# Kernel tuning notes

Hardware: AMD Instinct MI355X
Metric: run time of the kernel (lower is better)

## Reference

```python
import jax, jax.numpy as jnp
import numpy as np

VOCAB = 50257
EMB = 256
HID = 256
FORGET_BIAS = 1.0


def setup_inputs() -> dict:
    key = jax.random.key(0)
    ks = jax.random.split(key, 8)
    B, T = 16, 256
    s = 0.05
    return {
        "tokens": jax.random.randint(ks[0], (B, T), 0, VOCAB, dtype=jnp.int32),
        # embedding matrix init mimics tf.random_uniform(-1, 1)
        "emb": jax.random.uniform(ks[1], (VOCAB, EMB), jnp.float32, -1.0, 1.0),
        "W1": jax.random.normal(ks[2], (EMB + HID, 4 * HID), jnp.float32) * s,
        "b1": jnp.zeros((4 * HID,), jnp.float32),
        "W2": jax.random.normal(ks[3], (HID + HID, 4 * HID), jnp.float32) * s,
        "b2": jnp.zeros((4 * HID,), jnp.float32),
        "Wout": jax.random.normal(ks[4], (HID, VOCAB), jnp.float32) * s,
        "bout": jnp.zeros((VOCAB,), jnp.float32),
    }


def _lstm_cell(c, h, x, W, b):
    # BasicLSTMCell: gates = [x, h] @ W + b, split i, j, f, o
    g = jnp.concatenate([x, h], axis=-1) @ W + b
    i, j, f, o = jnp.split(g, 4, axis=-1)
    c_new = c * jax.nn.sigmoid(f + FORGET_BIAS) + jax.nn.sigmoid(i) * jnp.tanh(j)
    h_new = jnp.tanh(c_new) * jax.nn.sigmoid(o)
    return c_new, h_new


def reference(tokens, emb, W1, b1, W2, b2, Wout, bout):
    B, T = tokens.shape
    x = emb[tokens]                 # [B, T, EMB] embedding lookup
    x_tm = jnp.swapaxes(x, 0, 1)    # [T, B, EMB] time-major for scan

    def step(carry, xt):
        c1, h1, c2, h2 = carry
        c1, h1 = _lstm_cell(c1, h1, xt, W1, b1)
        c2, h2 = _lstm_cell(c2, h2, h1, W2, b2)
        return (c1, h1, c2, h2), h2

    z = jnp.zeros((B, HID), x.dtype)
    _, hs = jax.lax.scan(step, (z, z, z, z), x_tm)  # hs: [T, B, HID]
    hs = jnp.swapaxes(hs, 0, 1).reshape(-1, HID)    # [B*T, HID] (batch-major flatten as in tf.reshape)
    logits = hs @ Wout + bout                        # [B*T, VOCAB]
    return logits
```

## Files before the change

### kernel.cpp

```cpp
#include <hip/hip_runtime.h>
#include <hip/hip_bf16.h>
#include <stdint.h>

#define BB 16
#define TT 256
#define HH 256
#define EE 256
#define GG 1024
#define VV 50257
#define NN 4096

typedef unsigned short u16;
typedef __attribute__((ext_vector_type(8))) short short8;
typedef __attribute__((ext_vector_type(4))) float f32x4;

__device__ __forceinline__ float sigm(float x){
    float e = __builtin_amdgcn_exp2f(fminf(-x*1.44269504f, 60.0f));
    return 1.0f/(1.0f+e);
}
__device__ __forceinline__ float tanha(float x){
    float e = __builtin_amdgcn_exp2f(fminf(x*2.885390082f, 60.0f));
    return (e-1.0f)/(e+1.0f);
}
__device__ __forceinline__ u16 f2bf(float f){
    uint32_t u = __float_as_uint(f);
    u = (u + 0x7FFFu + ((u>>16)&1u)) >> 16;
    return (u16)u;
}
__device__ __forceinline__ void st16_coh(u16* p, u16 v){
    __hip_atomic_store(p, v, __ATOMIC_RELAXED, __HIP_MEMORY_SCOPE_AGENT);
}
__device__ __forceinline__ uint32_t poll_pair(const uint32_t* p){
    uint32_t v = __hip_atomic_load(p, __ATOMIC_RELAXED, __HIP_MEMORY_SCOPE_AGENT);
    while ((v & 0xFFFFu) == 0xFFFFu || (v >> 16) == 0xFFFFu){
        __builtin_amdgcn_s_sleep(1);
        v = __hip_atomic_load(p, __ATOMIC_RELAXED, __HIP_MEMORY_SCOPE_AGENT);
    }
    return v;
}
__device__ __forceinline__ void gl_lds16(const void* g, void* s){
    __builtin_amdgcn_global_load_lds((const __attribute__((address_space(1))) unsigned int*)g,
                                     (__attribute__((address_space(3))) unsigned int*)s, 16, 0, 0);
}

__global__ __launch_bounds__(256) void g1_kernel(const int* __restrict__ tok, const float* __restrict__ emb,
                                                 const float* __restrict__ W1, const float* __restrict__ b1,
                                                 float* __restrict__ G1t){
    __shared__ float xs[64*64];
    __shared__ float wsm[64*64];
    int n0 = blockIdx.x * 64;
    int g0 = blockIdx.y * 64;
    int tid = threadIdx.x;
    int sl = tid & 63;
    int kk = (tid >> 6) * 16;
    int mytok = tok[n0 + sl];
    float acc[4][4] = {};
    int ni = tid & 15, gi = tid >> 4;
    for (int kc = 0; kc < 4; ++kc){
        int k0 = kc*64;
        __syncthreads();
        #pragma unroll
        for (int i4 = 0; i4 < 4; ++i4){
            float4 xv = *(const float4*)(&emb[(size_t)mytok*EE + k0 + kk + i4*4]);
            xs[(kk+i4*4+0)*64 + sl] = xv.x;
            xs[(kk+i4*4+1)*64 + sl] = xv.y;
            xs[(kk+i4*4+2)*64 + sl] = xv.z;
            xs[(kk+i4*4+3)*64 + sl] = xv.w;
        }
        #pragma unroll
        for (int i = 0; i < 16; ++i){
            wsm[(kk+i)*64 + sl] = W1[(size_t)(k0+kk+i)*GG + g0 + sl];
        }
        __syncthreads();
        for (int k = 0; k < 64; ++k){
            float4 av = *(const float4*)(&xs[k*64 + ni*4]);
            float4 bv = *(const float4*)(&wsm[k*64 + gi*4]);
            float a_[4] = {av.x, av.y, av.z, av.w};
            float b_[4] = {bv.x, bv.y, bv.z, bv.w};
            #pragma unroll
            for (int i = 0; i < 4; ++i)
                #pragma unroll
                for (int j = 0; j < 4; ++j)
                    acc[i][j] += a_[i]*b_[j];
        }
    }
    #pragma unroll
    for (int i = 0; i < 4; ++i){
        int n = n0 + ni*4 + i;
        int b = n >> 8;
        int tt_ = n & 255;
        float4 o;
        o.x = acc[i][0] + b1[g0+gi*4+0];
        o.y = acc[i][1] + b1[g0+gi*4+1];
        o.z = acc[i][2] + b1[g0+gi*4+2];
        o.w = acc[i][3] + b1[g0+gi*4+3];
        *(float4*)(&G1t[(size_t)(tt_*16 + b)*GG + g0 + gi*4]) = o;
    }
}

__global__ __launch_bounds__(1024) void persist_kernel(
        const float* __restrict__ G1t, const float* __restrict__ W1,
        const float* __restrict__ W2, const float* __restrict__ b2,
        const float* __restrict__ Wout, u16* __restrict__ WoutT,
        u16* __restrict__ h1y, u16* __restrict__ h2b){
    __shared__ __align__(16) char smem[12288];
    const int bid = blockIdx.x;
    const int tid = threadIdx.x;

    if (bid >= 96){
        u16* tile = (u16*)smem;
        const int r = tid >> 4, i = tid & 15;
        for (int tau = bid - 96; tau < 786*4; tau += 128){
            int ky = tau / 786;
            int nx = tau - ky*786;
            int n0 = nx*64, k0 = ky*64;
            #pragma unroll
            for (int jj = 0; jj < 4; ++jj){
                int n = n0 + i*4 + jj;
                float f = (n < VV) ? Wout[(size_t)(k0 + r)*VV + n] : 0.0f;
                tile[(i*4 + jj)*66 + r] = f2bf(f);
            }
            __syncthreads();
            {
                int kl = i*4;
                uint2 v;
                v.x = (uint32_t)tile[r*66 + kl+0] | ((uint32_t)tile[r*66 + kl+1] << 16);
                v.y = (uint32_t)tile[r*66 + kl+2] | ((uint32_t)tile[r*66 + kl+3] << 16);
                *(uint2*)(&WoutT[(size_t)(n0 + r)*256 + k0 + kl]) = v;
            }
            __syncthreads();
        }
        return;
    }

    const int g  = bid & 7;
    const int rr = bid >> 3;
    const int l  = tid & 63;
    const int wv = tid >> 6;
    uint32_t* h1y32 = (uint32_t*)h1y;
    uint32_t* h2b32 = (uint32_t*)h2b;

    if (rr < 4){
        const int r1 = rr;
        const int gate = wv >> 2, usub = wv & 3;
        const int colw = gate*HH + 64*r1 + 16*usub;
        short8 wf[8];
        {
            const int col = colw + (l & 15);
            const int kb = (l >> 4) << 3;
            #pragma unroll
            for (int kk = 0; kk < 8; ++kk){
                short8 s;
                #pragma unroll
                for (int j = 0; j < 8; ++j)
                    s[j] = (short)f2bf(W1[(size_t)(HH + kk*32 + kb + j)*GG + col]);
                wf[kk] = s;
            }
        }
        u16*      hA   = (u16*)smem;
        uint32_t* hA32 = (uint32_t*)smem;
        float* gm = (float*)(smem + 1024);
        float creg = 0.f;
        const int au = tid >> 1, ab = tid & 1;

        for (int t = 0; t < TT; ++t){
            float c0 = 0.f, c1 = 0.f;
            if (l < 16){
                c0 = G1t[((size_t)t*BB + 2*g + 0)*GG + colw + l];
                c1 = G1t[((size_t)t*BB + 2*g + 1)*GG + colw + l];
            }
            f32x4 acc = {c0, c1, 0.f, 0.f};
            if (t > 0){
                if (tid < 256){
                    int b = tid >> 7, p = tid & 127;
                    hA32[b*128 + p] = poll_pair(&h1y32[(((size_t)(t-1)*8 + g)*2 + b)*128 + p]);
                }
                __syncthreads();
                const u16* ap = hA + (l & 1)*256 + ((l >> 4) << 3);
                #pragma unroll
                for (int kk = 0; kk < 8; ++kk)
                    acc = __builtin_amdgcn_mfma_f32_16x16x32_bf16(
                            *(const short8*)(ap + kk*32), wf[kk], acc, 0, 0, 0);
            }
            if (l < 16){
                gm[(gate*64 + usub*16 + l)*2 + 0] = acc[0];
                gm[(gate*64 + usub*16 + l)*2 + 1] = acc[1];
            }
            __syncthreads();
            if (tid < 128){
                float gi_ = gm[(0*64 + au)*2 + ab];
                float gj_ = gm[(1*64 + au)*2 + ab];
                float gf_ = gm[(2*64 + au)*2 + ab];
                float go_ = gm[(3*64 + au)*2 + ab];
                float cn = creg * sigm(gf_ + 1.0f) + sigm(gi_)*tanha(gj_);
                float hn = tanha(cn)*sigm(go_);
                creg = cn;
                st16_coh(&h1y[(((size_t)t*8 + g)*2 + ab)*256 + 64*r1 + au], f2bf(hn));
            }
            __syncthreads();
        }
    } else {
        const int r2 = rr - 4;
        const int nt = wv >> 1, kh = wv & 1;
        const int gate = nt >> 1, usub = nt & 1;
        const int colw = gate*HH + 32*r2 + 16*usub;
        short8 wf[8];
        {
            const int col = colw + (l & 15);
            const int kb = (l >> 4) << 3;
            #pragma unroll
            for (int kk = 0; kk < 8; ++kk){
                short8 s;
                #pragma unroll
                for (int j = 0; j < 8; ++j)
                    s[j] = (short)f2bf(W2[(size_t)(kh*256 + kk*32 + kb + j)*GG + col]);
                wf[kk] = s;
            }
        }
        u16*      uB   = (u16*)smem;
        uint32_t* uB32 = (uint32_t*)smem;
        float* gm = (float*)(smem + 2048);
        float creg = 0.f;
        const int au = tid >> 1, ab = tid & 1;
        float bv0 = 0.f, bv1 = 0.f, bv2 = 0.f, bv3 = 0.f;
        if (tid < 64){
            bv0 = b2[0*HH + 32*r2 + au];
            bv1 = b2[1*HH + 32*r2 + au];
            bv2 = b2[2*HH + 32*r2 + au];
            bv3 = b2[3*HH + 32*r2 + au];
        }

        for (int tt = 0; tt < TT; ++tt){
            if (tid < 512){
                int b = tid >> 8, q = tid & 255;
                uint32_t v;
                if (q < 128)
                    v = poll_pair(&h1y32[(((size_t)tt*8 + g)*2 + b)*128 + q]);
                else if (tt > 0)
                    v = poll_pair(&h2b32[((size_t)(2*g + b)*TT + (tt-1))*128 + (q - 128)]);
                else
                    v = 0;
                uB32[b*256 + q] = v;
            }
            __syncthreads();
            f32x4 acc = {0.f, 0.f, 0.f, 0.f};
            const u16* ap = uB + (l & 1)*512 + kh*256 + ((l >> 4) << 3);
            #pragma unroll
            for (int kk = 0; kk < 8; ++kk)
                acc = __builtin_amdgcn_mfma_f32_16x16x32_bf16(
                        *(const short8*)(ap + kk*32), wf[kk], acc, 0, 0, 0);
            if (l < 16){
                gm[((gate*32 + usub*16 + l)*2 + 0)*2 + kh] = acc[0];
                gm[((gate*32 + usub*16 + l)*2 + 1)*2 + kh] = acc[1];
            }
            __syncthreads();
            if (tid < 64){
                float gi_ = gm[((0*32 + au)*2 + ab)*2 + 0] + gm[((0*32 + au)*2 + ab)*2 + 1] + bv0;
                float gj_ = gm[((1*32 + au)*2 + ab)*2 + 0] + gm[((1*32 + au)*2 + ab)*2 + 1] + bv1;
                float gf_ = gm[((2*32 + au)*2 + ab)*2 + 0] + gm[((2*32 + au)*2 + ab)*2 + 1] + bv2;
                float go_ = gm[((3*32 + au)*2 + ab)*2 + 0] + gm[((3*32 + au)*2 + ab)*2 + 1] + bv3;
                float cn = creg * sigm(gf_ + 1.0f) + sigm(gi_)*tanha(gj_);
                float hn = tanha(cn)*sigm(go_);
                creg = cn;
                st16_coh(&h2b[((size_t)(2*g + ab)*TT + tt)*HH + 32*r2 + au], f2bf(hn));
            }
            __syncthreads();
        }
    }
}

__global__ __launch_bounds__(256) void out_gemm(const u16* __restrict__ A, const u16* __restrict__ Bt,
                                                const float* __restrict__ bout, float* __restrict__ out){
    __shared__ __align__(16) u16 lds[2][2][8192];
    const int bid = blockIdx.x;
    const int wg  = (bid & 7)*1572 + (bid >> 3);
    const int mb = wg & 31, nb = wg >> 5;
    const int m0 = mb*128, n0 = nb*128;
    const int tid = threadIdx.x;
    const int l = tid & 63;
    const int wv = tid >> 6;
    const int wm = wv >> 1, wn = wv & 1;
    const int lr = l & 15, lh = l >> 4;

    f32x4 acc[4][4];
    #pragma unroll
    for (int mf = 0; mf < 4; ++mf)
        #pragma unroll
        for (int nf = 0; nf < 4; ++nf) acc[mf][nf] = (f32x4){0.f,0.f,0.f,0.f};

    #define STAGE(c, k0) { \
        _Pragma("unroll") \
        for (int j = 0; j < 4; ++j){ \
            int f = j*256 + tid; \
            int row = f >> 3; \
            int kps = (f & 7) ^ (row & 7); \
            gl_lds16(A  + (size_t)(m0+row)*256 + (k0) + kps*8, (char*)&lds[c][0][0] + f*16); \
            gl_lds16(Bt + (size_t)(n0+row)*256 + (k0) + kps*8, (char*)&lds[c][1][0] + f*16); \
        } }

    STAGE(0, 0)
    __syncthreads();
    #pragma unroll
    for (int ks = 0; ks < 4; ++ks){
        const int cur = ks & 1;
        if (ks < 3) STAGE(cur^1, (ks+1)*64)
        const char* ab = (const char*)&lds[cur][0][0];
        const char* bbp = (const char*)&lds[cur][1][0];
        #pragma unroll
        for (int ksub = 0; ksub < 2; ++ksub){
            short8 af[4], bf[4];
            const int kp = ksub*4 + lh;
            #pragma unroll
            for (int mf = 0; mf < 4; ++mf){
                int row = wm*64 + mf*16 + lr;
                af[mf] = *(const short8*)(ab + row*128 + ((kp ^ (row&7)) << 4));
            }
            #pragma unroll
            for (int nf = 0; nf < 4; ++nf){
                int row = wn*64 + nf*16 + lr;
                bf[nf] = *(const short8*)(bbp + row*128 + ((kp ^ (row&7)) << 4));
            }
            #pragma unroll
            for (int mf = 0; mf < 4; ++mf)
                #pragma unroll
                for (int nf = 0; nf < 4; ++nf)
                    acc[mf][nf] = __builtin_amdgcn_mfma_f32_16x16x32_bf16(af[mf], bf[nf], acc[mf][nf], 0, 0, 0);
        }
        __syncthreads();
    }
    #undef STAGE

    float* ldsF = (float*)&lds[0][0][0];
    #pragma unroll
    for (int nf = 0; nf < 4; ++nf){
        int col = wn*64 + nf*16 + lr;
        int gcol = n0 + col;
        float bb2 = (gcol < VV) ? bout[gcol] : 0.0f;
        #pragma unroll
        for (int mf = 0; mf < 4; ++mf)
            #pragma unroll
            for (int r = 0; r < 4; ++r){
                int row = wm*64 + mf*16 + lh*4 + r;
                ldsF[row*128 + col] = acc[mf][nf][r] + bb2;
            }
    }
    __syncthreads();
    #pragma unroll
    for (int j = 0; j < 16; ++j){
        int f = j*256 + tid;
        int row = f >> 5;
        int c4 = (f & 31)*4;
        int gcol = n0 + c4;
        float4 v = *(const float4*)(ldsF + row*128 + c4);
        if (gcol + 3 < VV){
            *(float4*)(&out[(size_t)(m0+row)*VV + gcol]) = v;
        } else {
            #pragma unroll
            for (int e = 0; e < 4; ++e)
                if (gcol + e < VV) out[(size_t)(m0+row)*VV + gcol + e] = ((const float*)&v)[e];
        }
    }
}

extern "C" void kernel_launch(void* const* d_in, const int* in_sizes, int n_in,
                              void* d_out, int out_size, void* d_ws, size_t ws_size,
                              hipStream_t stream) {
    const int*   tok  = (const int*)d_in[0];
    const float* emb  = (const float*)d_in[1];
    const float* W1   = (const float*)d_in[2];
    const float* b1   = (const float*)d_in[3];
    const float* W2   = (const float*)d_in[4];
    const float* b2   = (const float*)d_in[5];
    const float* Wout = (const float*)d_in[6];
    const float* bout = (const float*)d_in[7];
    float* out = (float*)d_out;
    char* ws = (char*)d_ws;

    u16*   h1y   = (u16*)  (ws);
    u16*   h2b   = (u16*)  (ws + 2097152);
    float* G1t   = (float*)(ws + 4194304);
    u16*   WoutT = (u16*)  (ws + 4194304 + 16777216);

    hipMemsetAsync(ws, 0xFF, 4194304, stream);
    g1_kernel<<<dim3(64, 16), 256, 0, stream>>>(tok, emb, W1, b1, G1t);
    persist_kernel<<<224, 1024, 0, stream>>>(G1t, W1, W2, b2, Wout, WoutT, h1y, h2b);
    out_gemm<<<12576, 256, 0, stream>>>(h2b, WoutT, bout, out);
}
```

Baseline: 883.8 us.

## Retile output GEMM to 64x512 tiles with direct nontemporal stores; pack LSTM h stores

The output projection GEMM moves from 128x128 tiles to 64x512 tiles. Each wave owns 16 rows and 32 N-fragments, with K staged in 32-wide chunks. The LDS-staged epilogue is replaced by direct scalar nontemporal stores to the logits, and WoutT is padded to 50688 columns so the wider tiles stay in bounds. The LSTM recurrence splits its MFMA chain into two accumulators for more ILP, and each thread now handles two hidden units and writes them as one 32-bit coherent store, halving the number of coherent stores. The risk is that the scalar, only partly coalesced output stores and the higher register use (32 accumulators) could hurt the write-bandwidth-bound GEMM.

```diff
diff --git a/kernel.cpp b/kernel.cpp
--- a/kernel.cpp
+++ b/kernel.cpp
@@ -8,6 +8,7 @@
 #define EE 256
 #define GG 1024
 #define VV 50257
+#define NP 50688
 #define NN 4096
 
 typedef unsigned short u16;
@@ -27,7 +28,7 @@
     u = (u + 0x7FFFu + ((u>>16)&1u)) >> 16;
     return (u16)u;
 }
-__device__ __forceinline__ void st16_coh(u16* p, u16 v){
+__device__ __forceinline__ void st32_coh(uint32_t* p, uint32_t v){
     __hip_atomic_store(p, v, __ATOMIC_RELAXED, __HIP_MEMORY_SCOPE_AGENT);
 }
 __device__ __forceinline__ uint32_t poll_pair(const uint32_t* p){
@@ -110,9 +111,9 @@
     if (bid >= 96){
         u16* tile = (u16*)smem;
         const int r = tid >> 4, i = tid & 15;
-        for (int tau = bid - 96; tau < 786*4; tau += 128){
-            int ky = tau / 786;
-            int nx = tau - ky*786;
+        for (int tau = bid - 96; tau < 792*4; tau += 128){
+            int ky = tau / 792;
+            int nx = tau - ky*792;
             int n0 = nx*64, k0 = ky*64;
             #pragma unroll
             for (int jj = 0; jj < 4; ++jj){
@@ -160,8 +161,8 @@
         u16*      hA   = (u16*)smem;
         uint32_t* hA32 = (uint32_t*)smem;
         float* gm = (float*)(smem + 1024);
-        float creg = 0.f;
-        const int au = tid >> 1, ab = tid & 1;
+        const int ab = tid >> 5, ap_ = tid & 31;
+        float creg0 = 0.f, creg1 = 0.f;
 
         for (int t = 0; t < TT; ++t){
             float c0 = 0.f, c1 = 0.f;
@@ -176,26 +177,34 @@
                     hA32[b*128 + p] = poll_pair(&h1y32[(((size_t)(t-1)*8 + g)*2 + b)*128 + p]);
                 }
                 __syncthreads();
-                const u16* ap = hA + (l & 1)*256 + ((l >> 4) << 3);
+                const u16* app = hA + (l & 1)*256 + ((l >> 4) << 3);
+                f32x4 acc2 = {0.f, 0.f, 0.f, 0.f};
                 #pragma unroll
-                for (int kk = 0; kk < 8; ++kk)
-                    acc = __builtin_amdgcn_mfma_f32_16x16x32_bf16(
-                            *(const short8*)(ap + kk*32), wf[kk], acc, 0, 0, 0);
+                for (int kk = 0; kk < 4; ++kk){
+                    acc  = __builtin_amdgcn_mfma_f32_16x16x32_bf16(*(const short8*)(app + (2*kk  )*32), wf[2*kk  ], acc , 0, 0, 0);
+                    acc2 = __builtin_amdgcn_mfma_f32_16x16x32_bf16(*(const short8*)(app + (2*kk+1)*32), wf[2*kk+1], acc2, 0, 0, 0);
+                }
+                acc[0] += acc2[0];
+                acc[1] += acc2[1];
             }
             if (l < 16){
                 gm[(gate*64 + usub*16 + l)*2 + 0] = acc[0];
                 gm[(gate*64 + usub*16 + l)*2 + 1] = acc[1];
             }
             __syncthreads();
-            if (tid < 128){
-                float gi_ = gm[(0*64 + au)*2 + ab];
-                float gj_ = gm[(1*64 + au)*2 + ab];
-                float gf_ = gm[(2*64 + au)*2 + ab];
-                float go_ = gm[(3*64 + au)*2 + ab];
-                float cn = creg * sigm(gf_ + 1.0f) + sigm(gi_)*tanha(gj_);
-                float hn = tanha(cn)*sigm(go_);
-                creg = cn;
-                st16_coh(&h1y[(((size_t)t*8 + g)*2 + ab)*256 + 64*r1 + au], f2bf(hn));
+            if (tid < 64){
+                int u0 = 2*ap_, u1 = 2*ap_ + 1;
+                float gi0 = gm[(0*64 + u0)*2 + ab], gi1 = gm[(0*64 + u1)*2 + ab];
+                float gj0 = gm[(1*64 + u0)*2 + ab], gj1 = gm[(1*64 + u1)*2 + ab];
+                float gf0 = gm[(2*64 + u0)*2 + ab], gf1 = gm[(2*64 + u1)*2 + ab];
+                float go0 = gm[(3*64 + u0)*2 + ab], go1 = gm[(3*64 + u1)*2 + ab];
+                float cn0 = creg0 * sigm(gf0 + 1.0f) + sigm(gi0)*tanha(gj0);
+                float cn1 = creg1 * sigm(gf1 + 1.0f) + sigm(gi1)*tanha(gj1);
+                float hn0 = tanha(cn0)*sigm(go0);
+                float hn1 = tanha(cn1)*sigm(go1);
+                creg0 = cn0; creg1 = cn1;
+                uint32_t pk = (uint32_t)f2bf(hn0) | ((uint32_t)f2bf(hn1) << 16);
+                st32_coh(&h1y32[(((size_t)t*8 + g)*2 + ab)*128 + 32*r1 + ap_], pk);
             }
             __syncthreads();
         }
@@ -220,14 +229,15 @@
         u16*      uB   = (u16*)smem;
         uint32_t* uB32 = (uint32_t*)smem;
         float* gm = (float*)(smem + 2048);
-        float creg = 0.f;
-        const int au = tid >> 1, ab = tid & 1;
-        float bv0 = 0.f, bv1 = 0.f, bv2 = 0.f, bv3 = 0.f;
-        if (tid < 64){
-            bv0 = b2[0*HH + 32*r2 + au];
-            bv1 = b2[1*HH + 32*r2 + au];
-            bv2 = b2[2*HH + 32*r2 + au];
-            bv3 = b2[3*HH + 32*r2 + au];
+        const int ab = tid >> 4, ap_ = tid & 15;
+        float creg0 = 0.f, creg1 = 0.f;
+        float bvs[4][2];
+        if (tid < 32){
+            #pragma unroll
+            for (int gg = 0; gg < 4; ++gg){
+                bvs[gg][0] = b2[gg*HH + 32*r2 + 2*ap_];
+                bvs[gg][1] = b2[gg*HH + 32*r2 + 2*ap_ + 1];
+            }
         }
 
         for (int tt = 0; tt < TT; ++tt){
@@ -244,25 +254,37 @@
             }
             __syncthreads();
             f32x4 acc = {0.f, 0.f, 0.f, 0.f};
-            const u16* ap = uB + (l & 1)*512 + kh*256 + ((l >> 4) << 3);
-            #pragma unroll
-            for (int kk = 0; kk < 8; ++kk)
-                acc = __builtin_amdgcn_mfma_f32_16x16x32_bf16(
-                        *(const short8*)(ap + kk*32), wf[kk], acc, 0, 0, 0);
+            f32x4 acc2 = {0.f, 0.f, 0.f, 0.f};
+            const u16* app = uB + (l & 1)*512 + kh*256 + ((l >> 4) << 3);
+            #pragma unroll
+            for (int kk = 0; kk < 4; ++kk){
+                acc  = __builtin_amdgcn_mfma_f32_16x16x32_bf16(*(const short8*)(app + (2*kk  )*32), wf[2*kk  ], acc , 0, 0, 0);
+                acc2 = __builtin_amdgcn_mfma_f32_16x16x32_bf16(*(const short8*)(app + (2*kk+1)*32), wf[2*kk+1], acc2, 0, 0, 0);
+            }
+            acc[0] += acc2[0];
+            acc[1] += acc2[1];
             if (l < 16){
                 gm[((gate*32 + usub*16 + l)*2 + 0)*2 + kh] = acc[0];
                 gm[((gate*32 + usub*16 + l)*2 + 1)*2 + kh] = acc[1];
             }
             __syncthreads();
-            if (tid < 64){
-                float gi_ = gm[((0*32 + au)*2 + ab)*2 + 0] + gm[((0*32 + au)*2 + ab)*2 + 1] + bv0;
-                float gj_ = gm[((1*32 + au)*2 + ab)*2 + 0] + gm[((1*32 + au)*2 + ab)*2 + 1] + bv1;
-                float gf_ = gm[((2*32 + au)*2 + ab)*2 + 0] + gm[((2*32 + au)*2 + ab)*2 + 1] + bv2;
-                float go_ = gm[((3*32 + au)*2 + ab)*2 + 0] + gm[((3*32 + au)*2 + ab)*2 + 1] + bv3;
-                float cn = creg * sigm(gf_ + 1.0f) + sigm(gi_)*tanha(gj_);
-                float hn = tanha(cn)*sigm(go_);
-                creg = cn;
-                st16_coh(&h2b[((size_t)(2*g + ab)*TT + tt)*HH + 32*r2 + au], f2bf(hn));
+            if (tid < 32){
+                int u0 = 2*ap_, u1 = 2*ap_ + 1;
+                float gi0 = gm[((0*32 + u0)*2 + ab)*2 + 0] + gm[((0*32 + u0)*2 + ab)*2 + 1] + bvs[0][0];
+                float gi1 = gm[((0*32 + u1)*2 + ab)*2 + 0] + gm[((0*32 + u1)*2 + ab)*2 + 1] + bvs[0][1];
+                float gj0 = gm[((1*32 + u0)*2 + ab)*2 + 0] + gm[((1*32 + u0)*2 + ab)*2 + 1] + bvs[1][0];
+                float gj1 = gm[((1*32 + u1)*2 + ab)*2 + 0] + gm[((1*32 + u1)*2 + ab)*2 + 1] + bvs[1][1];
+                float gf0 = gm[((2*32 + u0)*2 + ab)*2 + 0] + gm[((2*32 + u0)*2 + ab)*2 + 1] + bvs[2][0];
+                float gf1 = gm[((2*32 + u1)*2 + ab)*2 + 0] + gm[((2*32 + u1)*2 + ab)*2 + 1] + bvs[2][1];
+                float go0 = gm[((3*32 + u0)*2 + ab)*2 + 0] + gm[((3*32 + u0)*2 + ab)*2 + 1] + bvs[3][0];
+                float go1 = gm[((3*32 + u1)*2 + ab)*2 + 0] + gm[((3*32 + u1)*2 + ab)*2 + 1] + bvs[3][1];
+                float cn0 = creg0 * sigm(gf0 + 1.0f) + sigm(gi0)*tanha(gj0);
+                float cn1 = creg1 * sigm(gf1 + 1.0f) + sigm(gi1)*tanha(gj1);
+                float hn0 = tanha(cn0)*sigm(go0);
+                float hn1 = tanha(cn1)*sigm(go1);
+                creg0 = cn0; creg1 = cn1;
+                uint32_t pk = (uint32_t)f2bf(hn0) | ((uint32_t)f2bf(hn1) << 16);
+                st32_coh(&h2b32[((size_t)(2*g + ab)*TT + tt)*128 + 16*r2 + ap_], pk);
             }
             __syncthreads();
         }
@@ -271,93 +293,65 @@
 
 __global__ __launch_bounds__(256) void out_gemm(const u16* __restrict__ A, const u16* __restrict__ Bt,
                                                 const float* __restrict__ bout, float* __restrict__ out){
-    __shared__ __align__(16) u16 lds[2][2][8192];
+    __shared__ __align__(16) u16 ldsA[2][2048];
+    __shared__ __align__(16) u16 ldsB[2][16384];
     const int bid = blockIdx.x;
-    const int wg  = (bid & 7)*1572 + (bid >> 3);
-    const int mb = wg & 31, nb = wg >> 5;
-    const int m0 = mb*128, n0 = nb*128;
+    const int wg  = (bid & 7)*792 + (bid >> 3);
+    const int mb = wg & 63, nb = wg >> 6;
+    const int m0 = mb*64, n0 = nb*512;
     const int tid = threadIdx.x;
     const int l = tid & 63;
     const int wv = tid >> 6;
-    const int wm = wv >> 1, wn = wv & 1;
     const int lr = l & 15, lh = l >> 4;
 
-    f32x4 acc[4][4];
+    f32x4 acc[32];
     #pragma unroll
-    for (int mf = 0; mf < 4; ++mf)
-        #pragma unroll
-        for (int nf = 0; nf < 4; ++nf) acc[mf][nf] = (f32x4){0.f,0.f,0.f,0.f};
+    for (int nf = 0; nf < 32; ++nf) acc[nf] = (f32x4){0.f,0.f,0.f,0.f};
 
     #define STAGE(c, k0) { \
+        { int f = tid; int row = f >> 2; int kp = f & 3; \
+          int kps = kp ^ (row & 3) ^ ((row >> 2) & 3); \
+          gl_lds16(A + (size_t)(m0+row)*256 + (k0) + kps*8, (char*)&ldsA[c][0] + f*16); } \
         _Pragma("unroll") \
-        for (int j = 0; j < 4; ++j){ \
-            int f = j*256 + tid; \
-            int row = f >> 3; \
-            int kps = (f & 7) ^ (row & 7); \
-            gl_lds16(A  + (size_t)(m0+row)*256 + (k0) + kps*8, (char*)&lds[c][0][0] + f*16); \
-            gl_lds16(Bt + (size_t)(n0+row)*256 + (k0) + kps*8, (char*)&lds[c][1][0] + f*16); \
-        } }
+        for (int j = 0; j < 8; ++j){ \
+            int f = j*256 + tid; int row = f >> 2; int kp = f & 3; \
+            int kps = kp ^ (row & 3) ^ ((row >> 2) & 3); \
+            gl_lds16(Bt + (size_t)(n0+row)*256 + (k0) + kps*8, (char*)&ldsB[c][0] + f*16); } \
+        }
 
     STAGE(0, 0)
     __syncthreads();
     #pragma unroll
-    for (int ks = 0; ks < 4; ++ks){
+    for (int ks = 0; ks < 8; ++ks){
         const int cur = ks & 1;
-        if (ks < 3) STAGE(cur^1, (ks+1)*64)
-        const char* ab = (const char*)&lds[cur][0][0];
-        const char* bbp = (const char*)&lds[cur][1][0];
+        if (ks < 7) STAGE(cur^1, (ks+1)*32)
+        short8 af;
+        {
+            int row = 16*wv + lr;
+            int up = lh ^ (row & 3) ^ ((row >> 2) & 3);
+            af = *(const short8*)((const char*)&ldsA[cur][0] + row*64 + up*16);
+        }
         #pragma unroll
-        for (int ksub = 0; ksub < 2; ++ksub){
-            short8 af[4], bf[4];
-            const int kp = ksub*4 + lh;
-            #pragma unroll
-            for (int mf = 0; mf < 4; ++mf){
-                int row = wm*64 + mf*16 + lr;
-                af[mf] = *(const short8*)(ab + row*128 + ((kp ^ (row&7)) << 4));
-            }
-            #pragma unroll
-            for (int nf = 0; nf < 4; ++nf){
-                int row = wn*64 + nf*16 + lr;
-                bf[nf] = *(const short8*)(bbp + row*128 + ((kp ^ (row&7)) << 4));
-            }
-            #pragma unroll
-            for (int mf = 0; mf < 4; ++mf)
-                #pragma unroll
-                for (int nf = 0; nf < 4; ++nf)
-                    acc[mf][nf] = __builtin_amdgcn_mfma_f32_16x16x32_bf16(af[mf], bf[nf], acc[mf][nf], 0, 0, 0);
+        for (int nf = 0; nf < 32; ++nf){
+            int row = nf*16 + lr;
+            int up = lh ^ (row & 3) ^ ((row >> 2) & 3);
+            short8 bf = *(const short8*)((const char*)&ldsB[cur][0] + row*64 + up*16);
+            acc[nf] = __builtin_amdgcn_mfma_f32_16x16x32_bf16(af, bf, acc[nf], 0, 0, 0);
         }
         __syncthreads();
     }
     #undef STAGE
 
-    float* ldsF = (float*)&lds[0][0][0];
     #pragma unroll
-    for (int nf = 0; nf < 4; ++nf){
-        int col = wn*64 + nf*16 + lr;
-        int gcol = n0 + col;
-        float bb2 = (gcol < VV) ? bout[gcol] : 0.0f;
-        #pragma unroll
-        for (int mf = 0; mf < 4; ++mf)
+    for (int nf = 0; nf < 32; ++nf){
+        int gcol = n0 + nf*16 + lr;
+        if (gcol < VV){
+            float bb = bout[gcol];
             #pragma unroll
             for (int r = 0; r < 4; ++r){
-                int row = wm*64 + mf*16 + lh*4 + r;
-                ldsF[row*128 + col] = acc[mf][nf][r] + bb2;
-            }
-    }
-    __syncthreads();
-    #pragma unroll
-    for (int j = 0; j < 16; ++j){
-        int f = j*256 + tid;
-        int row = f >> 5;
-        int c4 = (f & 31)*4;
-        int gcol = n0 + c4;
-        float4 v = *(const float4*)(ldsF + row*128 + c4);
-        if (gcol + 3 < VV){
-            *(float4*)(&out[(size_t)(m0+row)*VV + gcol]) = v;
-        } else {
-            #pragma unroll
-            for (int e = 0; e < 4; ++e)
-                if (gcol + e < VV) out[(size_t)(m0+row)*VV + gcol + e] = ((const float*)&v)[e];
+                int grow = m0 + 16*wv + lh*4 + r;
+                __builtin_nontemporal_store(acc[nf][r] + bb, &out[(size_t)grow*VV + gcol]);
+            }
         }
     }
 }
@@ -384,5 +378,5 @@
     hipMemsetAsync(ws, 0xFF, 4194304, stream);
     g1_kernel<<<dim3(64, 16), 256, 0, stream>>>(tok, emb, W1, b1, G1t);
     persist_kernel<<<224, 1024, 0, stream>>>(G1t, W1, W2, b2, Wout, WoutT, h1y, h2b);
-    out_gemm<<<12576, 256, 0, stream>>>(h2b, WoutT, bout, out);
-}
+    out_gemm<<<6336, 256, 0, stream>>>(h2b, WoutT, bout, out);
+}
```

Measured after the change: 1.363 ms. +54.2%, slower.

## Double-buffer recurrent LDS state to drop a barrier and pack h stores

Applied to the files above, without the earlier changes.

The LSTM recurrence kernels now double-buffer both the shared-memory h staging area and the gate scratch by timestep parity, which lets each step drop its trailing __syncthreads. Each cell-update thread now handles two hidden units and writes them as one packed 32-bit coherent store instead of two 16-bit ones, halving the number of cross-block publish stores. The MFMA accumulation is also split into two independent chains to shorten the dependency latency. This costs extra LDS and relies on parity buffering being enough to avoid write-after-read races between consecutive steps.

```diff
diff --git a/kernel.cpp b/kernel.cpp
--- a/kernel.cpp
+++ b/kernel.cpp
@@ -27,7 +27,7 @@
     u = (u + 0x7FFFu + ((u>>16)&1u)) >> 16;
     return (u16)u;
 }
-__device__ __forceinline__ void st16_coh(u16* p, u16 v){
+__device__ __forceinline__ void st32_coh(uint32_t* p, uint32_t v){
     __hip_atomic_store(p, v, __ATOMIC_RELAXED, __HIP_MEMORY_SCOPE_AGENT);
 }
 __device__ __forceinline__ uint32_t poll_pair(const uint32_t* p){
@@ -159,11 +159,12 @@
         }
         u16*      hA   = (u16*)smem;
         uint32_t* hA32 = (uint32_t*)smem;
-        float* gm = (float*)(smem + 1024);
-        float creg = 0.f;
-        const int au = tid >> 1, ab = tid & 1;
+        float*    gm   = (float*)(smem + 2048);
+        const int ab = tid >> 5, ap_ = tid & 31;
+        float creg0 = 0.f, creg1 = 0.f;
 
         for (int t = 0; t < TT; ++t){
+            const int pb = t & 1;
             float c0 = 0.f, c1 = 0.f;
             if (l < 16){
                 c0 = G1t[((size_t)t*BB + 2*g + 0)*GG + colw + l];
@@ -173,31 +174,38 @@
             if (t > 0){
                 if (tid < 256){
                     int b = tid >> 7, p = tid & 127;
-                    hA32[b*128 + p] = poll_pair(&h1y32[(((size_t)(t-1)*8 + g)*2 + b)*128 + p]);
+                    hA32[pb*256 + b*128 + p] = poll_pair(&h1y32[(((size_t)(t-1)*8 + g)*2 + b)*128 + p]);
                 }
                 __syncthreads();
-                const u16* ap = hA + (l & 1)*256 + ((l >> 4) << 3);
+                const u16* app = hA + pb*512 + (l & 1)*256 + ((l >> 4) << 3);
+                f32x4 acc2 = {0.f, 0.f, 0.f, 0.f};
                 #pragma unroll
-                for (int kk = 0; kk < 8; ++kk)
-                    acc = __builtin_amdgcn_mfma_f32_16x16x32_bf16(
-                            *(const short8*)(ap + kk*32), wf[kk], acc, 0, 0, 0);
+                for (int kk = 0; kk < 4; ++kk){
+                    acc  = __builtin_amdgcn_mfma_f32_16x16x32_bf16(*(const short8*)(app + (2*kk  )*32), wf[2*kk  ], acc , 0, 0, 0);
+                    acc2 = __builtin_amdgcn_mfma_f32_16x16x32_bf16(*(const short8*)(app + (2*kk+1)*32), wf[2*kk+1], acc2, 0, 0, 0);
+                }
+                acc[0] += acc2[0];
+                acc[1] += acc2[1];
             }
             if (l < 16){
-                gm[(gate*64 + usub*16 + l)*2 + 0] = acc[0];
-                gm[(gate*64 + usub*16 + l)*2 + 1] = acc[1];
+                gm[pb*512 + (gate*64 + usub*16 + l)*2 + 0] = acc[0];
+                gm[pb*512 + (gate*64 + usub*16 + l)*2 + 1] = acc[1];
             }
             __syncthreads();
-            if (tid < 128){
-                float gi_ = gm[(0*64 + au)*2 + ab];
-                float gj_ = gm[(1*64 + au)*2 + ab];
-                float gf_ = gm[(2*64 + au)*2 + ab];
-                float go_ = gm[(3*64 + au)*2 + ab];
-                float cn = creg * sigm(gf_ + 1.0f) + sigm(gi_)*tanha(gj_);
-                float hn = tanha(cn)*sigm(go_);
-                creg = cn;
-                st16_coh(&h1y[(((size_t)t*8 + g)*2 + ab)*256 + 64*r1 + au], f2bf(hn));
-            }
-            __syncthreads();
+            if (tid < 64){
+                int u0 = 2*ap_, u1 = 2*ap_ + 1;
+                float gi0 = gm[pb*512 + (0*64 + u0)*2 + ab], gi1 = gm[pb*512 + (0*64 + u1)*2 + ab];
+                float gj0 = gm[pb*512 + (1*64 + u0)*2 + ab], gj1 = gm[pb*512 + (1*64 + u1)*2 + ab];
+                float gf0 = gm[pb*512 + (2*64 + u0)*2 + ab], gf1 = gm[pb*512 + (2*64 + u1)*2 + ab];
+                float go0 = gm[pb*512 + (3*64 + u0)*2 + ab], go1 = gm[pb*512 + (3*64 + u1)*2 + ab];
+                float cn0 = creg0 * sigm(gf0 + 1.0f) + sigm(gi0)*tanha(gj0);
+                float cn1 = creg1 * sigm(gf1 + 1.0f) + sigm(gi1)*tanha(gj1);
+                float hn0 = tanha(cn0)*sigm(go0);
+                float hn1 = tanha(cn1)*sigm(go1);
+                creg0 = cn0; creg1 = cn1;
+                uint32_t pk = (uint32_t)f2bf(hn0) | ((uint32_t)f2bf(hn1) << 16);
+                st32_coh(&h1y32[(((size_t)t*8 + g)*2 + ab)*128 + 32*r1 + ap_], pk);
+            }
         }
     } else {
         const int r2 = rr - 4;
@@ -219,18 +227,20 @@
         }
         u16*      uB   = (u16*)smem;
         uint32_t* uB32 = (uint32_t*)smem;
-        float* gm = (float*)(smem + 2048);
-        float creg = 0.f;
-        const int au = tid >> 1, ab = tid & 1;
-        float bv0 = 0.f, bv1 = 0.f, bv2 = 0.f, bv3 = 0.f;
-        if (tid < 64){
-            bv0 = b2[0*HH + 32*r2 + au];
-            bv1 = b2[1*HH + 32*r2 + au];
-            bv2 = b2[2*HH + 32*r2 + au];
-            bv3 = b2[3*HH + 32*r2 + au];
+        float*    gm   = (float*)(smem + 4096);
+        const int ab = tid >> 4, ap_ = tid & 15;
+        float creg0 = 0.f, creg1 = 0.f;
+        float bvs[4][2];
+        if (tid < 32){
+            #pragma unroll
+            for (int gg = 0; gg < 4; ++gg){
+                bvs[gg][0] = b2[gg*HH + 32*r2 + 2*ap_];
+                bvs[gg][1] = b2[gg*HH + 32*r2 + 2*ap_ + 1];
+            }
         }
 
         for (int tt = 0; tt < TT; ++tt){
+            const int pb = tt & 1;
             if (tid < 512){
                 int b = tid >> 8, q = tid & 255;
                 uint32_t v;
@@ -240,31 +250,43 @@
                     v = poll_pair(&h2b32[((size_t)(2*g + b)*TT + (tt-1))*128 + (q - 128)]);
                 else
                     v = 0;
-                uB32[b*256 + q] = v;
+                uB32[pb*512 + b*256 + q] = v;
             }
             __syncthreads();
             f32x4 acc = {0.f, 0.f, 0.f, 0.f};
-            const u16* ap = uB + (l & 1)*512 + kh*256 + ((l >> 4) << 3);
-            #pragma unroll
-            for (int kk = 0; kk < 8; ++kk)
-                acc = __builtin_amdgcn_mfma_f32_16x16x32_bf16(
-                        *(const short8*)(ap + kk*32), wf[kk], acc, 0, 0, 0);
+            f32x4 acc2 = {0.f, 0.f, 0.f, 0.f};
+            const u16* app = uB + pb*1024 + (l & 1)*512 + kh*256 + ((l >> 4) << 3);
+            #pragma unroll
+            for (int kk = 0; kk < 4; ++kk){
+                acc  = __builtin_amdgcn_mfma_f32_16x16x32_bf16(*(const short8*)(app + (2*kk  )*32), wf[2*kk  ], acc , 0, 0, 0);
+                acc2 = __builtin_amdgcn_mfma_f32_16x16x32_bf16(*(const short8*)(app + (2*kk+1)*32), wf[2*kk+1], acc2, 0, 0, 0);
+            }
+            acc[0] += acc2[0];
+            acc[1] += acc2[1];
             if (l < 16){
-                gm[((gate*32 + usub*16 + l)*2 + 0)*2 + kh] = acc[0];
-                gm[((gate*32 + usub*16 + l)*2 + 1)*2 + kh] = acc[1];
+                gm[pb*512 + ((gate*32 + usub*16 + l)*2 + 0)*2 + kh] = acc[0];
+                gm[pb*512 + ((gate*32 + usub*16 + l)*2 + 1)*2 + kh] = acc[1];
             }
             __syncthreads();
-            if (tid < 64){
-                float gi_ = gm[((0*32 + au)*2 + ab)*2 + 0] + gm[((0*32 + au)*2 + ab)*2 + 1] + bv0;
-                float gj_ = gm[((1*32 + au)*2 + ab)*2 + 0] + gm[((1*32 + au)*2 + ab)*2 + 1] + bv1;
-                float gf_ = gm[((2*32 + au)*2 + ab)*2 + 0] + gm[((2*32 + au)*2 + ab)*2 + 1] + bv2;
-                float go_ = gm[((3*32 + au)*2 + ab)*2 + 0] + gm[((3*32 + au)*2 + ab)*2 + 1] + bv3;
-                float cn = creg * sigm(gf_ + 1.0f) + sigm(gi_)*tanha(gj_);
-                float hn = tanha(cn)*sigm(go_);
-                creg = cn;
-                st16_coh(&h2b[((size_t)(2*g + ab)*TT + tt)*HH + 32*r2 + au], f2bf(hn));
-            }
-            __syncthreads();
+            if (tid < 32){
+                int u0 = 2*ap_, u1 = 2*ap_ + 1;
+                const float* gp = gm + pb*512;
+                float gi0 = gp[((0*32 + u0)*2 + ab)*2 + 0] + gp[((0*32 + u0)*2 + ab)*2 + 1] + bvs[0][0];
+                float gi1 = gp[((0*32 + u1)*2 + ab)*2 + 0] + gp[((0*32 + u1)*2 + ab)*2 + 1] + bvs[0][1];
+                float gj0 = gp[((1*32 + u0)*2 + ab)*2 + 0] + gp[((1*32 + u0)*2 + ab)*2 + 1] + bvs[1][0];
+                float gj1 = gp[((1*32 + u1)*2 + ab)*2 + 0] + gp[((1*32 + u1)*2 + ab)*2 + 1] + bvs[1][1];
+                float gf0 = gp[((2*32 + u0)*2 + ab)*2 + 0] + gp[((2*32 + u0)*2 + ab)*2 + 1] + bvs[2][0];
+                float gf1 = gp[((2*32 + u1)*2 + ab)*2 + 0] + gp[((2*32 + u1)*2 + ab)*2 + 1] + bvs[2][1];
+                float go0 = gp[((3*32 + u0)*2 + ab)*2 + 0] + gp[((3*32 + u0)*2 + ab)*2 + 1] + bvs[3][0];
+                float go1 = gp[((3*32 + u1)*2 + ab)*2 + 0] + gp[((3*32 + u1)*2 + ab)*2 + 1] + bvs[3][1];
+                float cn0 = creg0 * sigm(gf0 + 1.0f) + sigm(gi0)*tanha(gj0);
+                float cn1 = creg1 * sigm(gf1 + 1.0f) + sigm(gi1)*tanha(gj1);
+                float hn0 = tanha(cn0)*sigm(go0);
+                float hn1 = tanha(cn1)*sigm(go1);
+                creg0 = cn0; creg1 = cn1;
+                uint32_t pk = (uint32_t)f2bf(hn0) | ((uint32_t)f2bf(hn1) << 16);
+                st32_coh(&h2b32[((size_t)(2*g + ab)*TT + tt)*128 + 16*r2 + ap_], pk);
+            }
         }
     }
 }
```

Result: slower. 946.3 us (+7.1%).
